# Kernel tuning notes

Hardware: AMD Instinct MI355X
Metric: run time of the kernel (lower is better)

The kernel has to match this reference:

```python
import jax, jax.numpy as jnp
import numpy as np

B, T, INPUT, H, NCLS = 16384, 64, 78, 8, 11

def setup_inputs() -> dict:
    key = jax.random.key(0)
    ks = jax.random.split(key, 9)
    s = lambda fan: 1.0 / np.sqrt(fan)
    return {
        "x":   jax.random.normal(ks[0], (B, T, INPUT), dtype=jnp.float32),
        "W_ih": jax.random.normal(ks[1], (4 * H, INPUT), dtype=jnp.float32) * s(H),
        "W_hh": jax.random.normal(ks[2], (4 * H, H), dtype=jnp.float32) * s(H),
        "b_ih": jax.random.normal(ks[3], (4 * H,), dtype=jnp.float32) * s(H),
        "b_hh": jax.random.normal(ks[4], (4 * H,), dtype=jnp.float32) * s(H),
        "W1":  jax.random.normal(ks[5], (16, H), dtype=jnp.float32) * s(H),
        "b1":  jax.random.normal(ks[6], (16,), dtype=jnp.float32) * s(H),
        "W2":  jax.random.normal(ks[7], (NCLS, 16), dtype=jnp.float32) * s(16),
        "b2":  jax.random.normal(ks[8], (NCLS,), dtype=jnp.float32) * s(16),
    }

def _lstm_last(x, W_ih, W_hh, b_ih, b_hh):
    # x: [B, T, INPUT]; PyTorch gate order i, f, g, o along the 4H axis.
    Bsz = x.shape[0]
    Hd = W_hh.shape[1]
    # Precompute input projections for all timesteps: [T, B, 4H]
    xg = jnp.einsum('bti,gi->tbg', x, W_ih) + (b_ih + b_hh)
    h0 = jnp.zeros((Bsz, Hd), dtype=x.dtype)
    c0 = jnp.zeros((Bsz, Hd), dtype=x.dtype)

    def step(carry, xg_t):
        h, c = carry
        gates = xg_t + h @ W_hh.T  # [B, 4H]
        i, f, g, o = jnp.split(gates, 4, axis=-1)
        i = jax.nn.sigmoid(i)
        f = jax.nn.sigmoid(f)
        g = jnp.tanh(g)
        o = jax.nn.sigmoid(o)
        c = f * c + i * g
        h = o * jnp.tanh(c)
        return (h, c), None

    (h, _), _ = jax.lax.scan(step, (h0, c0), xg)
    return h  # last hidden state == out[:, -1, :]

def reference(x, W_ih, W_hh, b_ih, b_hh, W1, b1, W2, b2):
    h = _lstm_last(x, W_ih, W_hh, b_ih, b_hh)      # [B, H]
    # dropout is identity in eval mode
    h = jax.nn.relu(h)
    h = h @ W1.T + b1                               # [B, 16]
    h = jax.nn.relu(h)
    h = h @ W2.T + b2                               # [B, num_classes]
    return jax.nn.softmax(h, axis=-1)
```

## Files before the change

kernel.cpp:

```cpp
#include <hip/hip_runtime.h>


#define B_SZ 16384
#define T_SZ 64
#define IN_SZ 78
#define H_SZ 8
#define G_SZ 32
#define NCLS 11
#define NB 32
#define TT 4
#define NTHREADS 256
#define ACT_STRIDE 33
#define ROW_STRIDE (T_SZ * IN_SZ)

__global__ __launch_bounds__(NTHREADS)
void lstm_fused(const float* __restrict__ x,
                const float* __restrict__ W_ih,
                const float* __restrict__ W_hh,
                const float* __restrict__ b_ih,
                const float* __restrict__ b_hh,
                const float* __restrict__ W1,
                const float* __restrict__ b1,
                const float* __restrict__ W2,
                const float* __restrict__ b2,
                float* __restrict__ out)
{
    __shared__ float x_lds[TT * NB * IN_SZ];
    __shared__ float WihT[IN_SZ * G_SZ];
    __shared__ float WhhT[H_SZ * G_SZ];
    __shared__ float actT[G_SZ * ACT_STRIDE];
    __shared__ float hT[H_SZ * NB];
    __shared__ float bias_l[G_SZ];
    __shared__ float W1_l[16 * 8];
    __shared__ float b1_l[16];
    __shared__ float W2_l[NCLS * 16];
    __shared__ float b2_l[NCLS];

    const int tid = threadIdx.x;
    const int rowbase = blockIdx.x * NB;

    for (int i = tid; i < IN_SZ * G_SZ; i += NTHREADS) {
        int g = i / IN_SZ, k = i - g * IN_SZ;
        WihT[k * G_SZ + g] = W_ih[i];
    }
    for (int i = tid; i < G_SZ * H_SZ; i += NTHREADS) {
        int g = i / H_SZ, j = i - g * H_SZ;
        WhhT[j * G_SZ + g] = W_hh[i];
    }
    if (tid < G_SZ)      bias_l[tid] = b_ih[tid] + b_hh[tid];
    if (tid < 128)       W1_l[tid] = W1[tid];
    if (tid < 16)        b1_l[tid] = b1[tid];
    if (tid < NCLS * 16) W2_l[tid] = W2[tid];
    if (tid < NCLS)      b2_l[tid] = b2[tid];
    hT[tid] = 0.0f;
    __syncthreads();

    const int rg = tid & 15;
    const int gg = tid >> 4;
    const int r0 = rg * 2;
    const int g0 = gg * 2;
    const float bias0 = bias_l[g0];
    const float bias1 = bias_l[g0 + 1];
    const bool isTanh = (g0 >= 16) && (g0 < 24);

    const int oj = tid >> 5;
    const int orr = tid & 31;
    float c_reg = 0.0f;

    const int row_seed = tid / IN_SZ;
    const int k_seed = tid - row_seed * IN_SZ;
    const int goff_seed = row_seed * ROW_STRIDE + k_seed;
    const float* xblk = x + (size_t)rowbase * ROW_STRIDE;

    for (int it = 0; it < T_SZ / TT; ++it) {
        const int t0 = it * TT;
        const float* xit = xblk + t0 * IN_SZ;

        {
            int k = k_seed;
            int row = row_seed;
            int goff = goff_seed;
            #pragma unroll
            for (int j = 0; j < 39; ++j) {
                x_lds[tid + j * NTHREADS] = xit[goff];
                k += 22; row += 3; goff += 3 * ROW_STRIDE + 22;
                if (k >= IN_SZ) { k -= IN_SZ; row += 1; goff += ROW_STRIDE - IN_SZ; }
                if (row >= NB)  { row -= NB; goff += IN_SZ - NB * ROW_STRIDE; }
            }
        }
        __syncthreads();

        float acc[TT][2][2];
        #pragma unroll
        for (int tt = 0; tt < TT; ++tt) {
            acc[tt][0][0] = bias0; acc[tt][0][1] = bias1;
            acc[tt][1][0] = bias0; acc[tt][1][1] = bias1;
        }

        #pragma unroll 3
        for (int k0 = 0; k0 < IN_SZ; k0 += 2) {
            float2 w0 = *(const float2*)&WihT[(k0    ) * G_SZ + g0];
            float2 w1 = *(const float2*)&WihT[(k0 + 1) * G_SZ + g0];
            #pragma unroll
            for (int tt = 0; tt < TT; ++tt) {
                #pragma unroll
                for (int rr = 0; rr < 2; ++rr) {
                    float2 xv = *(const float2*)&x_lds[(tt * NB + r0 + rr) * IN_SZ + k0];
                    acc[tt][rr][0] += xv.x * w0.x + xv.y * w1.x;
                    acc[tt][rr][1] += xv.x * w0.y + xv.y * w1.y;
                }
            }
        }

        #pragma unroll
        for (int tt = 0; tt < TT; ++tt) {
            float rec[2][2] = {{0.f, 0.f}, {0.f, 0.f}};
            #pragma unroll
            for (int j = 0; j < H_SZ; ++j) {
                float2 hv = *(const float2*)&hT[j * NB + r0];
                float2 wv = *(const float2*)&WhhT[j * G_SZ + g0];
                rec[0][0] += hv.x * wv.x;  rec[0][1] += hv.x * wv.y;
                rec[1][0] += hv.y * wv.x;  rec[1][1] += hv.y * wv.y;
            }
            #pragma unroll
            for (int rr = 0; rr < 2; ++rr) {
                #pragma unroll
                for (int g2 = 0; g2 < 2; ++g2) {
                    float v = acc[tt][rr][g2] + rec[rr][g2];
                    float arg = isTanh ? 2.0f * v : v;
                    float s = 1.0f / (1.0f + __expf(-arg));
                    float a = isTanh ? (2.0f * s - 1.0f) : s;
                    actT[(g0 + g2) * ACT_STRIDE + (r0 + rr)] = a;
                }
            }
            __syncthreads();
            {
                float iv = actT[(oj     ) * ACT_STRIDE + orr];
                float fv = actT[(oj +  8) * ACT_STRIDE + orr];
                float gv = actT[(oj + 16) * ACT_STRIDE + orr];
                float ov = actT[(oj + 24) * ACT_STRIDE + orr];
                c_reg = fv * c_reg + iv * gv;
                float s = 1.0f / (1.0f + __expf(-2.0f * c_reg));
                float th = 2.0f * s - 1.0f;
                hT[oj * NB + orr] = ov * th;
            }
            __syncthreads();
        }
    }

    float* z1T = actT;
    {
        const int r = tid & 31;
        const int uu = tid >> 5;
        float hr[H_SZ];
        #pragma unroll
        for (int j = 0; j < H_SZ; ++j) hr[j] = fmaxf(hT[j * NB + r], 0.0f);
        #pragma unroll
        for (int u2 = 0; u2 < 2; ++u2) {
            int u = uu * 2 + u2;
            float z = b1_l[u];
            #pragma unroll
            for (int j = 0; j < H_SZ; ++j) z += hr[j] * W1_l[u * 8 + j];
            z1T[u * ACT_STRIDE + r] = fmaxf(z, 0.0f);
        }
    }
    __syncthreads();
    if (tid < NB) {
        const int r = tid;
        float z1v[16];
        #pragma unroll
        for (int u = 0; u < 16; ++u) z1v[u] = z1T[u * ACT_STRIDE + r];
        float z2[NCLS];
        float m = -1e30f;
        #pragma unroll
        for (int c = 0; c < NCLS; ++c) {
            float v = b2_l[c];
            #pragma unroll
            for (int u = 0; u < 16; ++u) v += z1v[u] * W2_l[c * 16 + u];
            z2[c] = v;
            m = fmaxf(m, v);
        }
        float s = 0.0f;
        #pragma unroll
        for (int c = 0; c < NCLS; ++c) { z2[c] = __expf(z2[c] - m); s += z2[c]; }
        float inv = 1.0f / s;
        float* op = out + (size_t)(rowbase + r) * NCLS;
        #pragma unroll
        for (int c = 0; c < NCLS; ++c) op[c] = z2[c] * inv;
    }
}

extern "C" void kernel_launch(void* const* d_in, const int* in_sizes, int n_in,
                              void* d_out, int out_size, void* d_ws, size_t ws_size,
                              hipStream_t stream) {
    const float* x    = (const float*)d_in[0];
    const float* W_ih = (const float*)d_in[1];
    const float* W_hh = (const float*)d_in[2];
    const float* b_ih = (const float*)d_in[3];
    const float* b_hh = (const float*)d_in[4];
    const float* W1   = (const float*)d_in[5];
    const float* b1   = (const float*)d_in[6];
    const float* W2   = (const float*)d_in[7];
    const float* b2   = (const float*)d_in[8];
    float* outp = (float*)d_out;

    lstm_fused<<<dim3(B_SZ / NB), dim3(NTHREADS), 0, stream>>>(
        x, W_ih, W_hh, b_ih, b_hh, W1, b1, W2, b2, outp);
}
```

Before: 574.3 us.

## Restructure LSTM kernel with wave-shuffle recurrence, register prefetch, and smaller row tiles

Rows per block drop from 32 to 16, and each thread now owns one row and two gates. The recurrent gate exchange and hidden-state broadcast move from LDS with two block barriers per timestep to cross-lane shuffles inside a wavefront, with W_hh held in registers. The next x tile is prefetched into registers with vector loads while the current tile's recurrence runs, and packed two-float math is used. This is meant to remove per-step barriers and overlap global loads with compute, at the cost of more shuffles, more register pressure, and twice as many blocks each reloading the weights.

```diff
diff --git a/kernel.cpp b/kernel.cpp
--- a/kernel.cpp
+++ b/kernel.cpp
@@ -1,19 +1,31 @@
 #include <hip/hip_runtime.h>
 
+
+typedef float v2f __attribute__((ext_vector_type(2)));
 
 #define B_SZ 16384
 #define T_SZ 64
 #define IN_SZ 78
 #define H_SZ 8
-#define G_SZ 32
 #define NCLS 11
-#define NB 32
+#define NB 16
 #define TT 4
 #define NTHREADS 256
-#define ACT_STRIDE 33
-#define ROW_STRIDE (T_SZ * IN_SZ)
-
-__global__ __launch_bounds__(NTHREADS)
+#define NITER (T_SZ / TT)
+#define K2 (IN_SZ / 2)
+#define XTILE (TT * NB * K2)
+#define ROWSTR (T_SZ * IN_SZ)
+
+__device__ __forceinline__ float sigm(float x) { return 1.0f / (1.0f + __expf(-x)); }
+
+__device__ __forceinline__ v2f shfl2(v2f v, int srcLane) {
+    v2f r;
+    r.x = __shfl(v.x, srcLane, 64);
+    r.y = __shfl(v.y, srcLane, 64);
+    return r;
+}
+
+__global__ __launch_bounds__(NTHREADS, 4)
 void lstm_fused(const float* __restrict__ x,
                 const float* __restrict__ W_ih,
                 const float* __restrict__ W_hh,
@@ -25,158 +37,207 @@
                 const float* __restrict__ b2,
                 float* __restrict__ out)
 {
-    __shared__ float x_lds[TT * NB * IN_SZ];
-    __shared__ float WihT[IN_SZ * G_SZ];
-    __shared__ float WhhT[H_SZ * G_SZ];
-    __shared__ float actT[G_SZ * ACT_STRIDE];
-    __shared__ float hT[H_SZ * NB];
-    __shared__ float bias_l[G_SZ];
-    __shared__ float W1_l[16 * 8];
-    __shared__ float b1_l[16];
-    __shared__ float W2_l[NCLS * 16];
-    __shared__ float b2_l[NCLS];
+    __shared__ v2f   x2[XTILE];
+    __shared__ float WihT[IN_SZ * 32];
+    __shared__ float z1s[NB][17];
 
     const int tid = threadIdx.x;
-    const int rowbase = blockIdx.x * NB;
-
-    for (int i = tid; i < IN_SZ * G_SZ; i += NTHREADS) {
-        int g = i / IN_SZ, k = i - g * IN_SZ;
-        WihT[k * G_SZ + g] = W_ih[i];
-    }
-    for (int i = tid; i < G_SZ * H_SZ; i += NTHREADS) {
-        int g = i / H_SZ, j = i - g * H_SZ;
-        WhhT[j * G_SZ + g] = W_hh[i];
-    }
-    if (tid < G_SZ)      bias_l[tid] = b_ih[tid] + b_hh[tid];
-    if (tid < 128)       W1_l[tid] = W1[tid];
-    if (tid < 16)        b1_l[tid] = b1[tid];
-    if (tid < NCLS * 16) W2_l[tid] = W2[tid];
-    if (tid < NCLS)      b2_l[tid] = b2[tid];
-    hT[tid] = 0.0f;
+    const int gg  = tid & 15;
+    const int r   = tid >> 4;
+    const int lane = tid & 63;
+    const int typeIdx = gg >> 2;
+    const bool isT = (typeIdx == 2);
+    const int pr = gg & 3;
+    const int laneBase = (lane & 0x30) | pr;
+    const int laneQ    = lane & ~3;
+
+    const size_t rowbase = (size_t)blockIdx.x * NB;
+    const float* xb = x + rowbase * ROWSTR;
+
+    const int G0 = 2 * gg, G1 = 2 * gg + 1;
+    v2f bias; bias.x = b_ih[G0] + b_hh[G0]; bias.y = b_ih[G1] + b_hh[G1];
+    v2f Whh_r[H_SZ];
+    #pragma unroll
+    for (int j = 0; j < H_SZ; ++j) {
+        Whh_r[j].x = W_hh[G0 * H_SZ + j];
+        Whh_r[j].y = W_hh[G1 * H_SZ + j];
+    }
+
+    int goff[10];
+    {
+        int trow = tid / K2;
+        int k2   = tid - trow * K2;
+        #pragma unroll
+        for (int j = 0; j < 10; ++j) {
+            goff[j] = (trow & (NB - 1)) * ROWSTR + (trow >> 4) * IN_SZ + 2 * k2;
+            trow += 6; k2 += 22;
+            if (k2 >= K2) { k2 -= K2; trow += 1; }
+        }
+    }
+
+    v2f xv[10];
+    #pragma unroll
+    for (int j = 0; j < 9; ++j) xv[j] = *(const v2f*)&xb[goff[j]];
+    if (tid < 192)              xv[9] = *(const v2f*)&xb[goff[9]];
+
+    float wtmp[10];
+    #pragma unroll
+    for (int j = 0; j < 10; ++j) {
+        int p = tid + j * NTHREADS;
+        if (j < 9 || tid < 192) wtmp[j] = W_ih[p];
+    }
+    #pragma unroll
+    for (int j = 0; j < 10; ++j) {
+        int p = tid + j * NTHREADS;
+        if (j < 9 || tid < 192) {
+            int g = p / IN_SZ, k = p - g * IN_SZ;
+            WihT[k * 32 + g] = wtmp[j];
+        }
+    }
+    #pragma unroll
+    for (int j = 0; j < 9; ++j) x2[tid + j * NTHREADS] = xv[j];
+    if (tid < 192)              x2[tid + 9 * NTHREADS] = xv[9];
     __syncthreads();
 
-    const int rg = tid & 15;
-    const int gg = tid >> 4;
-    const int r0 = rg * 2;
-    const int g0 = gg * 2;
-    const float bias0 = bias_l[g0];
-    const float bias1 = bias_l[g0 + 1];
-    const bool isTanh = (g0 >= 16) && (g0 < 24);
-
-    const int oj = tid >> 5;
-    const int orr = tid & 31;
-    float c_reg = 0.0f;
-
-    const int row_seed = tid / IN_SZ;
-    const int k_seed = tid - row_seed * IN_SZ;
-    const int goff_seed = row_seed * ROW_STRIDE + k_seed;
-    const float* xblk = x + (size_t)rowbase * ROW_STRIDE;
-
-    for (int it = 0; it < T_SZ / TT; ++it) {
-        const int t0 = it * TT;
-        const float* xit = xblk + t0 * IN_SZ;
-
-        {
-            int k = k_seed;
-            int row = row_seed;
-            int goff = goff_seed;
+    v2f c2;   c2.x = 0.0f; c2.y = 0.0f;
+    v2f hq[4];
+    #pragma unroll
+    for (int q = 0; q < 4; ++q) { hq[q].x = 0.0f; hq[q].y = 0.0f; }
+
+    v2f acc[TT];
+    #pragma unroll
+    for (int tt = 0; tt < TT; ++tt) acc[tt] = bias;
+    #pragma unroll 3
+    for (int k0 = 0; k0 < IN_SZ; k0 += 2) {
+        v2f w0 = *(const v2f*)&WihT[(k0    ) * 32 + G0];
+        v2f w1 = *(const v2f*)&WihT[(k0 + 1) * 32 + G0];
+        #pragma unroll
+        for (int tt = 0; tt < TT; ++tt) {
+            v2f xk = x2[(tt * NB + r) * K2 + (k0 >> 1)];
+            v2f sx; sx.x = xk.x; sx.y = xk.x;
+            v2f sy; sy.x = xk.y; sy.y = xk.y;
+            acc[tt] += sx * w0;
+            acc[tt] += sy * w1;
+        }
+    }
+
+    for (int it = 1; it < NITER; ++it) {
+        const float* xit = xb + it * (TT * IN_SZ);
+        #pragma unroll
+        for (int j = 0; j < 9; ++j) xv[j] = *(const v2f*)&xit[goff[j]];
+        if (tid < 192)              xv[9] = *(const v2f*)&xit[goff[9]];
+
+        #pragma unroll
+        for (int tt = 0; tt < TT; ++tt) {
+            v2f v = acc[tt];
             #pragma unroll
-            for (int j = 0; j < 39; ++j) {
-                x_lds[tid + j * NTHREADS] = xit[goff];
-                k += 22; row += 3; goff += 3 * ROW_STRIDE + 22;
-                if (k >= IN_SZ) { k -= IN_SZ; row += 1; goff += ROW_STRIDE - IN_SZ; }
-                if (row >= NB)  { row -= NB; goff += IN_SZ - NB * ROW_STRIDE; }
+            for (int q = 0; q < 4; ++q) {
+                v2f hx; hx.x = hq[q].x; hx.y = hq[q].x;
+                v2f hy; hy.x = hq[q].y; hy.y = hq[q].y;
+                v += hx * Whh_r[2 * q];
+                v += hy * Whh_r[2 * q + 1];
             }
-        }
+            v2f a;
+            {
+                float ax = isT ? 2.0f * v.x : v.x;
+                float ay = isT ? 2.0f * v.y : v.y;
+                float sxv = sigm(ax), syv = sigm(ay);
+                a.x = isT ? 2.0f * sxv - 1.0f : sxv;
+                a.y = isT ? 2.0f * syv - 1.0f : syv;
+            }
+            v2f i2 = shfl2(a, laneBase);
+            v2f f2 = shfl2(a, laneBase + 4);
+            v2f g2 = shfl2(a, laneBase + 8);
+            v2f o2 = shfl2(a, laneBase + 12);
+            c2 = f2 * c2 + i2 * g2;
+            v2f th;
+            th.x = 2.0f * sigm(2.0f * c2.x) - 1.0f;
+            th.y = 2.0f * sigm(2.0f * c2.y) - 1.0f;
+            v2f h2 = o2 * th;
+            hq[0] = shfl2(h2, laneQ);
+            hq[1] = shfl2(h2, laneQ | 1);
+            hq[2] = shfl2(h2, laneQ | 2);
+            hq[3] = shfl2(h2, laneQ | 3);
+        }
+
         __syncthreads();
-
-        float acc[TT][2][2];
-        #pragma unroll
-        for (int tt = 0; tt < TT; ++tt) {
-            acc[tt][0][0] = bias0; acc[tt][0][1] = bias1;
-            acc[tt][1][0] = bias0; acc[tt][1][1] = bias1;
-        }
-
+        #pragma unroll
+        for (int j = 0; j < 9; ++j) x2[tid + j * NTHREADS] = xv[j];
+        if (tid < 192)              x2[tid + 9 * NTHREADS] = xv[9];
+        __syncthreads();
+
+        #pragma unroll
+        for (int tt = 0; tt < TT; ++tt) acc[tt] = bias;
         #pragma unroll 3
         for (int k0 = 0; k0 < IN_SZ; k0 += 2) {
-            float2 w0 = *(const float2*)&WihT[(k0    ) * G_SZ + g0];
-            float2 w1 = *(const float2*)&WihT[(k0 + 1) * G_SZ + g0];
+            v2f w0 = *(const v2f*)&WihT[(k0    ) * 32 + G0];
+            v2f w1 = *(const v2f*)&WihT[(k0 + 1) * 32 + G0];
             #pragma unroll
             for (int tt = 0; tt < TT; ++tt) {
-                #pragma unroll
-                for (int rr = 0; rr < 2; ++rr) {
-                    float2 xv = *(const float2*)&x_lds[(tt * NB + r0 + rr) * IN_SZ + k0];
-                    acc[tt][rr][0] += xv.x * w0.x + xv.y * w1.x;
-                    acc[tt][rr][1] += xv.x * w0.y + xv.y * w1.y;
-                }
+                v2f xk = x2[(tt * NB + r) * K2 + (k0 >> 1)];
+                v2f sx; sx.x = xk.x; sx.y = xk.x;
+                v2f sy; sy.x = xk.y; sy.y = xk.y;
+                acc[tt] += sx * w0;
+                acc[tt] += sy * w1;
             }
         }
-
-        #pragma unroll
-        for (int tt = 0; tt < TT; ++tt) {
-            float rec[2][2] = {{0.f, 0.f}, {0.f, 0.f}};
-            #pragma unroll
-            for (int j = 0; j < H_SZ; ++j) {
-                float2 hv = *(const float2*)&hT[j * NB + r0];
-                float2 wv = *(const float2*)&WhhT[j * G_SZ + g0];
-                rec[0][0] += hv.x * wv.x;  rec[0][1] += hv.x * wv.y;
-                rec[1][0] += hv.y * wv.x;  rec[1][1] += hv.y * wv.y;
-            }
-            #pragma unroll
-            for (int rr = 0; rr < 2; ++rr) {
-                #pragma unroll
-                for (int g2 = 0; g2 < 2; ++g2) {
-                    float v = acc[tt][rr][g2] + rec[rr][g2];
-                    float arg = isTanh ? 2.0f * v : v;
-                    float s = 1.0f / (1.0f + __expf(-arg));
-                    float a = isTanh ? (2.0f * s - 1.0f) : s;
-                    actT[(g0 + g2) * ACT_STRIDE + (r0 + rr)] = a;
-                }
-            }
-            __syncthreads();
-            {
-                float iv = actT[(oj     ) * ACT_STRIDE + orr];
-                float fv = actT[(oj +  8) * ACT_STRIDE + orr];
-                float gv = actT[(oj + 16) * ACT_STRIDE + orr];
-                float ov = actT[(oj + 24) * ACT_STRIDE + orr];
-                c_reg = fv * c_reg + iv * gv;
-                float s = 1.0f / (1.0f + __expf(-2.0f * c_reg));
-                float th = 2.0f * s - 1.0f;
-                hT[oj * NB + orr] = ov * th;
-            }
-            __syncthreads();
-        }
-    }
-
-    float* z1T = actT;
+    }
+
+    #pragma unroll
+    for (int tt = 0; tt < TT; ++tt) {
+        v2f v = acc[tt];
+        #pragma unroll
+        for (int q = 0; q < 4; ++q) {
+            v2f hx; hx.x = hq[q].x; hx.y = hq[q].x;
+            v2f hy; hy.x = hq[q].y; hy.y = hq[q].y;
+            v += hx * Whh_r[2 * q];
+            v += hy * Whh_r[2 * q + 1];
+        }
+        v2f a;
+        {
+            float ax = isT ? 2.0f * v.x : v.x;
+            float ay = isT ? 2.0f * v.y : v.y;
+            float sxv = sigm(ax), syv = sigm(ay);
+            a.x = isT ? 2.0f * sxv - 1.0f : sxv;
+            a.y = isT ? 2.0f * syv - 1.0f : syv;
+        }
+        v2f i2 = shfl2(a, laneBase);
+        v2f f2 = shfl2(a, laneBase + 4);
+        v2f g2 = shfl2(a, laneBase + 8);
+        v2f o2 = shfl2(a, laneBase + 12);
+        c2 = f2 * c2 + i2 * g2;
+        v2f th;
+        th.x = 2.0f * sigm(2.0f * c2.x) - 1.0f;
+        th.y = 2.0f * sigm(2.0f * c2.y) - 1.0f;
+        v2f h2 = o2 * th;
+        hq[0] = shfl2(h2, laneQ);
+        hq[1] = shfl2(h2, laneQ | 1);
+        hq[2] = shfl2(h2, laneQ | 2);
+        hq[3] = shfl2(h2, laneQ | 3);
+    }
+
     {
-        const int r = tid & 31;
-        const int uu = tid >> 5;
-        float hr[H_SZ];
-        #pragma unroll
-        for (int j = 0; j < H_SZ; ++j) hr[j] = fmaxf(hT[j * NB + r], 0.0f);
-        #pragma unroll
-        for (int u2 = 0; u2 < 2; ++u2) {
-            int u = uu * 2 + u2;
-            float z = b1_l[u];
-            #pragma unroll
-            for (int j = 0; j < H_SZ; ++j) z += hr[j] * W1_l[u * 8 + j];
-            z1T[u * ACT_STRIDE + r] = fmaxf(z, 0.0f);
-        }
+        float z1 = b1[gg];
+        #pragma unroll
+        for (int q = 0; q < 4; ++q) {
+            z1 += fmaxf(hq[q].x, 0.0f) * W1[gg * H_SZ + 2 * q];
+            z1 += fmaxf(hq[q].y, 0.0f) * W1[gg * H_SZ + 2 * q + 1];
+        }
+        z1s[r][gg] = fmaxf(z1, 0.0f);
     }
     __syncthreads();
     if (tid < NB) {
-        const int r = tid;
+        const int row = tid;
         float z1v[16];
         #pragma unroll
-        for (int u = 0; u < 16; ++u) z1v[u] = z1T[u * ACT_STRIDE + r];
+        for (int u = 0; u < 16; ++u) z1v[u] = z1s[row][u];
         float z2[NCLS];
         float m = -1e30f;
         #pragma unroll
         for (int c = 0; c < NCLS; ++c) {
-            float v = b2_l[c];
+            float v = b2[c];
             #pragma unroll
-            for (int u = 0; u < 16; ++u) v += z1v[u] * W2_l[c * 16 + u];
+            for (int u = 0; u < 16; ++u) v += z1v[u] * W2[c * 16 + u];
             z2[c] = v;
             m = fmaxf(m, v);
         }
@@ -184,7 +245,7 @@
         #pragma unroll
         for (int c = 0; c < NCLS; ++c) { z2[c] = __expf(z2[c] - m); s += z2[c]; }
         float inv = 1.0f / s;
-        float* op = out + (size_t)(rowbase + r) * NCLS;
+        float* op = out + (rowbase + row) * NCLS;
         #pragma unroll
         for (int c = 0; c < NCLS; ++c) op[c] = z2[c] * inv;
     }
```

Measured after the change: 505.5 us. -12.0%, faster.

## Rewrite LSTM kernel with in-register recurrence via DPP lane exchange

Applied to the files above, without the earlier changes.

Each block now handles 16 rows instead of 32. Each group of 16 lanes owns one batch row: a lane holds two gates of one type, and the hidden state and gate values move between lanes with DPP quad permutes instead of shared memory. This removes the two barriers per timestep. The global loads of x for the next time tile now run while the recurrent steps of the current tile execute (register prefetch), and the launch bounds request higher occupancy. The risks are more register pressure, twice as many blocks with weight setup repeated in each, and correctness that depends on the DPP lane mapping.

```diff
diff --git a/kernel.cpp b/kernel.cpp
--- a/kernel.cpp
+++ b/kernel.cpp
@@ -1,19 +1,34 @@
 #include <hip/hip_runtime.h>
 
+
+typedef float v2f __attribute__((ext_vector_type(2)));
 
 #define B_SZ 16384
 #define T_SZ 64
 #define IN_SZ 78
 #define H_SZ 8
-#define G_SZ 32
 #define NCLS 11
-#define NB 32
+#define NB 16
 #define TT 4
 #define NTHREADS 256
-#define ACT_STRIDE 33
-#define ROW_STRIDE (T_SZ * IN_SZ)
-
-__global__ __launch_bounds__(NTHREADS)
+#define NITER (T_SZ / TT)
+#define ROWSTR (T_SZ * IN_SZ)
+#define ROWF (TT * IN_SZ)
+#define TILE_F4 (NB * ROWF / 4)
+
+__device__ __forceinline__ float sigm(float x) { return 1.0f / (1.0f + __expf(-x)); }
+
+template<int CTRL>
+__device__ __forceinline__ float dpp_f(float x) {
+    return __int_as_float(__builtin_amdgcn_update_dpp(
+        0, __float_as_int(x), CTRL, 0xF, 0xF, true));
+}
+template<int CTRL>
+__device__ __forceinline__ v2f dpp2(v2f v) {
+    v2f r; r.x = dpp_f<CTRL>(v.x); r.y = dpp_f<CTRL>(v.y); return r;
+}
+
+__global__ __launch_bounds__(NTHREADS, 4)
 void lstm_fused(const float* __restrict__ x,
                 const float* __restrict__ W_ih,
                 const float* __restrict__ W_hh,
@@ -25,158 +40,178 @@
                 const float* __restrict__ b2,
                 float* __restrict__ out)
 {
-    __shared__ float x_lds[TT * NB * IN_SZ];
-    __shared__ float WihT[IN_SZ * G_SZ];
-    __shared__ float WhhT[H_SZ * G_SZ];
-    __shared__ float actT[G_SZ * ACT_STRIDE];
-    __shared__ float hT[H_SZ * NB];
-    __shared__ float bias_l[G_SZ];
-    __shared__ float W1_l[16 * 8];
-    __shared__ float b1_l[16];
-    __shared__ float W2_l[NCLS * 16];
-    __shared__ float b2_l[NCLS];
-
-    const int tid = threadIdx.x;
-    const int rowbase = blockIdx.x * NB;
-
-    for (int i = tid; i < IN_SZ * G_SZ; i += NTHREADS) {
-        int g = i / IN_SZ, k = i - g * IN_SZ;
-        WihT[k * G_SZ + g] = W_ih[i];
-    }
-    for (int i = tid; i < G_SZ * H_SZ; i += NTHREADS) {
-        int g = i / H_SZ, j = i - g * H_SZ;
-        WhhT[j * G_SZ + g] = W_hh[i];
-    }
-    if (tid < G_SZ)      bias_l[tid] = b_ih[tid] + b_hh[tid];
-    if (tid < 128)       W1_l[tid] = W1[tid];
-    if (tid < 16)        b1_l[tid] = b1[tid];
-    if (tid < NCLS * 16) W2_l[tid] = W2[tid];
-    if (tid < NCLS)      b2_l[tid] = b2[tid];
-    hT[tid] = 0.0f;
+    __shared__ float x2f[NB * ROWF];
+    __shared__ float Wq[39 * 16 * 4];
+    __shared__ float z1s[NB][17];
+
+    const int tid  = threadIdx.x;
+    const int type = tid & 3;
+    const int pr   = (tid >> 2) & 3;
+    const int rr   = tid >> 4;
+    const int u    = tid & 15;
+    const bool isT = (type == 2);
+
+    const size_t rowbase = (size_t)blockIdx.x * NB;
+    const float* xb = x + rowbase * ROWSTR;
+    const float4* xb4 = (const float4*)xb;
+
+    const int G0 = type * 8 + 2 * pr;
+    const int G1 = G0 + 1;
+    v2f bias; bias.x = b_ih[G0] + b_hh[G0]; bias.y = b_ih[G1] + b_hh[G1];
+    float4 WhhP[4];
+    #pragma unroll
+    for (int m = 0; m < 4; ++m) {
+        int p = pr ^ m;
+        WhhP[m].x = W_hh[G0 * H_SZ + 2 * p];
+        WhhP[m].y = W_hh[G0 * H_SZ + 2 * p + 1];
+        WhhP[m].z = W_hh[G1 * H_SZ + 2 * p];
+        WhhP[m].w = W_hh[G1 * H_SZ + 2 * p + 1];
+    }
+
+    int og[5];
+    {
+        int r0 = tid / IN_SZ;
+        int q  = tid - r0 * IN_SZ;
+        int oo = r0 * 1248 + q;
+        #pragma unroll
+        for (int j = 0; j < 5; ++j) {
+            og[j] = oo;
+            q += 22; oo += 3766;
+            if (q >= IN_SZ) { q -= IN_SZ; oo += 1170; }
+        }
+    }
+
+    float4 xv[5];
+    #pragma unroll
+    for (int j = 0; j < 4; ++j) xv[j] = xb4[og[j]];
+    if (tid < 224)              xv[4] = xb4[og[4]];
+
+    for (int i = tid; i < 39 * 64; i += NTHREADS) {
+        int e = i & 3, gl = (i >> 2) & 15, kp = i >> 6;
+        int ty = gl & 3, pp = gl >> 2;
+        int G = ty * 8 + 2 * pp + (e >> 1);
+        int k = 2 * kp + (e & 1);
+        Wq[i] = W_ih[G * IN_SZ + k];
+    }
+
+    float4* x2_4 = (float4*)x2f;
+    #pragma unroll
+    for (int j = 0; j < 4; ++j) x2_4[tid + j * NTHREADS] = xv[j];
+    if (tid < 224)              x2_4[tid + 4 * NTHREADS] = xv[4];
     __syncthreads();
 
-    const int rg = tid & 15;
-    const int gg = tid >> 4;
-    const int r0 = rg * 2;
-    const int g0 = gg * 2;
-    const float bias0 = bias_l[g0];
-    const float bias1 = bias_l[g0 + 1];
-    const bool isTanh = (g0 >= 16) && (g0 < 24);
-
-    const int oj = tid >> 5;
-    const int orr = tid & 31;
-    float c_reg = 0.0f;
-
-    const int row_seed = tid / IN_SZ;
-    const int k_seed = tid - row_seed * IN_SZ;
-    const int goff_seed = row_seed * ROW_STRIDE + k_seed;
-    const float* xblk = x + (size_t)rowbase * ROW_STRIDE;
-
-    for (int it = 0; it < T_SZ / TT; ++it) {
-        const int t0 = it * TT;
-        const float* xit = xblk + t0 * IN_SZ;
-
+    v2f c2; c2.x = 0.f; c2.y = 0.f;
+    v2f hrot[4];
+    #pragma unroll
+    for (int m = 0; m < 4; ++m) { hrot[m].x = 0.f; hrot[m].y = 0.f; }
+
+    const v2f*    x2v = (const v2f*)x2f;
+    const float4* wq4 = (const float4*)Wq;
+    float accx[TT], accy[TT];
+
+    #pragma unroll
+    for (int tt = 0; tt < TT; ++tt) { accx[tt] = bias.x; accy[tt] = bias.y; }
+    #pragma unroll 13
+    for (int kp = 0; kp < 39; ++kp) {
+        float4 wv = wq4[kp * 16 + u];
+        #pragma unroll
+        for (int tt = 0; tt < TT; ++tt) {
+            v2f xk = x2v[rr * 156 + tt * 39 + kp];
+            accx[tt] = fmaf(xk.x, wv.x, accx[tt]);
+            accx[tt] = fmaf(xk.y, wv.y, accx[tt]);
+            accy[tt] = fmaf(xk.x, wv.z, accy[tt]);
+            accy[tt] = fmaf(xk.y, wv.w, accy[tt]);
+        }
+    }
+
+    auto lstm_step = [&](float vx, float vy) {
+        #pragma unroll
+        for (int m = 0; m < 4; ++m) {
+            vx = fmaf(hrot[m].x, WhhP[m].x, vx);
+            vx = fmaf(hrot[m].y, WhhP[m].y, vx);
+            vy = fmaf(hrot[m].x, WhhP[m].z, vy);
+            vy = fmaf(hrot[m].y, WhhP[m].w, vy);
+        }
+        v2f a;
         {
-            int k = k_seed;
-            int row = row_seed;
-            int goff = goff_seed;
-            #pragma unroll
-            for (int j = 0; j < 39; ++j) {
-                x_lds[tid + j * NTHREADS] = xit[goff];
-                k += 22; row += 3; goff += 3 * ROW_STRIDE + 22;
-                if (k >= IN_SZ) { k -= IN_SZ; row += 1; goff += ROW_STRIDE - IN_SZ; }
-                if (row >= NB)  { row -= NB; goff += IN_SZ - NB * ROW_STRIDE; }
-            }
-        }
+            float ax = isT ? 2.0f * vx : vx;
+            float ay = isT ? 2.0f * vy : vy;
+            float sx = sigm(ax), sy = sigm(ay);
+            a.x = isT ? 2.0f * sx - 1.0f : sx;
+            a.y = isT ? 2.0f * sy - 1.0f : sy;
+        }
+        v2f i2 = dpp2<0x00>(a);
+        v2f f2 = dpp2<0x55>(a);
+        v2f g2 = dpp2<0xAA>(a);
+        v2f o2 = dpp2<0xFF>(a);
+        c2.x = fmaf(f2.x, c2.x, i2.x * g2.x);
+        c2.y = fmaf(f2.y, c2.y, i2.y * g2.y);
+        v2f th;
+        th.x = 2.0f * sigm(2.0f * c2.x) - 1.0f;
+        th.y = 2.0f * sigm(2.0f * c2.y) - 1.0f;
+        v2f h2; h2.x = o2.x * th.x; h2.y = o2.y * th.y;
+        hrot[0] = h2;
+        hrot[1] = dpp2<0x141>(h2);
+        hrot[2] = dpp2<0x128>(h2);
+        hrot[3] = dpp2<0x140>(h2);
+    };
+
+    for (int it = 1; it < NITER; ++it) {
+        const float4* xit4 = xb4 + it * 78;
+        #pragma unroll
+        for (int j = 0; j < 4; ++j) xv[j] = xit4[og[j]];
+        if (tid < 224)              xv[4] = xit4[og[4]];
+
+        #pragma unroll
+        for (int tt = 0; tt < TT; ++tt) lstm_step(accx[tt], accy[tt]);
+
         __syncthreads();
-
-        float acc[TT][2][2];
-        #pragma unroll
-        for (int tt = 0; tt < TT; ++tt) {
-            acc[tt][0][0] = bias0; acc[tt][0][1] = bias1;
-            acc[tt][1][0] = bias0; acc[tt][1][1] = bias1;
-        }
-
-        #pragma unroll 3
-        for (int k0 = 0; k0 < IN_SZ; k0 += 2) {
-            float2 w0 = *(const float2*)&WihT[(k0    ) * G_SZ + g0];
-            float2 w1 = *(const float2*)&WihT[(k0 + 1) * G_SZ + g0];
+        #pragma unroll
+        for (int j = 0; j < 4; ++j) x2_4[tid + j * NTHREADS] = xv[j];
+        if (tid < 224)              x2_4[tid + 4 * NTHREADS] = xv[4];
+        __syncthreads();
+
+        #pragma unroll
+        for (int tt = 0; tt < TT; ++tt) { accx[tt] = bias.x; accy[tt] = bias.y; }
+        #pragma unroll 13
+        for (int kp = 0; kp < 39; ++kp) {
+            float4 wv = wq4[kp * 16 + u];
             #pragma unroll
             for (int tt = 0; tt < TT; ++tt) {
-                #pragma unroll
-                for (int rr = 0; rr < 2; ++rr) {
-                    float2 xv = *(const float2*)&x_lds[(tt * NB + r0 + rr) * IN_SZ + k0];
-                    acc[tt][rr][0] += xv.x * w0.x + xv.y * w1.x;
-                    acc[tt][rr][1] += xv.x * w0.y + xv.y * w1.y;
-                }
+                v2f xk = x2v[rr * 156 + tt * 39 + kp];
+                accx[tt] = fmaf(xk.x, wv.x, accx[tt]);
+                accx[tt] = fmaf(xk.y, wv.y, accx[tt]);
+                accy[tt] = fmaf(xk.x, wv.z, accy[tt]);
+                accy[tt] = fmaf(xk.y, wv.w, accy[tt]);
             }
         }
-
-        #pragma unroll
-        for (int tt = 0; tt < TT; ++tt) {
-            float rec[2][2] = {{0.f, 0.f}, {0.f, 0.f}};
-            #pragma unroll
-            for (int j = 0; j < H_SZ; ++j) {
-                float2 hv = *(const float2*)&hT[j * NB + r0];
-                float2 wv = *(const float2*)&WhhT[j * G_SZ + g0];
-                rec[0][0] += hv.x * wv.x;  rec[0][1] += hv.x * wv.y;
-                rec[1][0] += hv.y * wv.x;  rec[1][1] += hv.y * wv.y;
-            }
-            #pragma unroll
-            for (int rr = 0; rr < 2; ++rr) {
-                #pragma unroll
-                for (int g2 = 0; g2 < 2; ++g2) {
-                    float v = acc[tt][rr][g2] + rec[rr][g2];
-                    float arg = isTanh ? 2.0f * v : v;
-                    float s = 1.0f / (1.0f + __expf(-arg));
-                    float a = isTanh ? (2.0f * s - 1.0f) : s;
-                    actT[(g0 + g2) * ACT_STRIDE + (r0 + rr)] = a;
-                }
-            }
-            __syncthreads();
-            {
-                float iv = actT[(oj     ) * ACT_STRIDE + orr];
-                float fv = actT[(oj +  8) * ACT_STRIDE + orr];
-                float gv = actT[(oj + 16) * ACT_STRIDE + orr];
-                float ov = actT[(oj + 24) * ACT_STRIDE + orr];
-                c_reg = fv * c_reg + iv * gv;
-                float s = 1.0f / (1.0f + __expf(-2.0f * c_reg));
-                float th = 2.0f * s - 1.0f;
-                hT[oj * NB + orr] = ov * th;
-            }
-            __syncthreads();
-        }
-    }
-
-    float* z1T = actT;
+    }
+    #pragma unroll
+    for (int tt = 0; tt < TT; ++tt) lstm_step(accx[tt], accy[tt]);
+
     {
-        const int r = tid & 31;
-        const int uu = tid >> 5;
-        float hr[H_SZ];
-        #pragma unroll
-        for (int j = 0; j < H_SZ; ++j) hr[j] = fmaxf(hT[j * NB + r], 0.0f);
-        #pragma unroll
-        for (int u2 = 0; u2 < 2; ++u2) {
-            int u = uu * 2 + u2;
-            float z = b1_l[u];
-            #pragma unroll
-            for (int j = 0; j < H_SZ; ++j) z += hr[j] * W1_l[u * 8 + j];
-            z1T[u * ACT_STRIDE + r] = fmaxf(z, 0.0f);
-        }
+        float z1 = b1[u];
+        #pragma unroll
+        for (int m = 0; m < 4; ++m) {
+            int p = pr ^ m;
+            z1 += fmaxf(hrot[m].x, 0.0f) * W1[u * H_SZ + 2 * p];
+            z1 += fmaxf(hrot[m].y, 0.0f) * W1[u * H_SZ + 2 * p + 1];
+        }
+        z1s[rr][u] = fmaxf(z1, 0.0f);
     }
     __syncthreads();
     if (tid < NB) {
-        const int r = tid;
+        const int row = tid;
         float z1v[16];
         #pragma unroll
-        for (int u = 0; u < 16; ++u) z1v[u] = z1T[u * ACT_STRIDE + r];
+        for (int uu = 0; uu < 16; ++uu) z1v[uu] = z1s[row][uu];
         float z2[NCLS];
         float m = -1e30f;
         #pragma unroll
         for (int c = 0; c < NCLS; ++c) {
-            float v = b2_l[c];
+            float v = b2[c];
             #pragma unroll
-            for (int u = 0; u < 16; ++u) v += z1v[u] * W2_l[c * 16 + u];
+            for (int uu = 0; uu < 16; ++uu) v += z1v[uu] * W2[c * 16 + uu];
             z2[c] = v;
             m = fmaxf(m, v);
         }
@@ -184,7 +219,7 @@
         #pragma unroll
         for (int c = 0; c < NCLS; ++c) { z2[c] = __expf(z2[c] - m); s += z2[c]; }
         float inv = 1.0f / s;
-        float* op = out + (size_t)(rowbase + r) * NCLS;
+        float* op = out + (rowbase + row) * NCLS;
         #pragma unroll
         for (int c = 0; c < NCLS; ++c) op[c] = z2[c] * inv;
     }
```

Result: faster. 544.6 us (-5.2%).
